# Performance work log

Hardware: AMD Instinct MI355X
Metric: run time of the kernel (lower is better)

Reference implementation:

```python
import jax, jax.numpy as jnp
import numpy as np

D_MODEL = 1024
N_HEADS = 16
HEAD_DIM = D_MODEL // N_HEADS
D_FF = 4 * D_MODEL
SEQ = 2048
BATCH = 2
EPS = 1e-6


def setup_inputs() -> dict:
    key = jax.random.key(0)
    ks = jax.random.split(key, 8)
    s = 0.02
    return {
        "x": jax.random.normal(ks[0], (SEQ, BATCH, D_MODEL), dtype=jnp.float32),
        "g1": jnp.ones((D_MODEL,), dtype=jnp.float32),                # norm1 weight
        "g2": jnp.ones((D_MODEL,), dtype=jnp.float32),                # norm2 weight
        "Wq": jax.random.normal(ks[1], (N_HEADS, D_MODEL, HEAD_DIM), dtype=jnp.float32) * s,
        "Wk": jax.random.normal(ks[2], (N_HEADS, D_MODEL, HEAD_DIM), dtype=jnp.float32) * s,
        "Wv": jax.random.normal(ks[3], (N_HEADS, D_MODEL, HEAD_DIM), dtype=jnp.float32) * s,
        "Wo": jax.random.normal(ks[4], (D_MODEL, D_MODEL), dtype=jnp.float32) * s,
        "W1": jax.random.normal(ks[5], (D_MODEL, D_FF), dtype=jnp.float32) * s,
        "W2": jax.random.normal(ks[6], (D_FF, D_MODEL), dtype=jnp.float32) * s,
    }


def _rmsnorm(x, g):
    rms = jnp.sqrt(jnp.mean(x * x, axis=-1, keepdims=True) + EPS)
    return g * (x / rms)


def _block(x, g1, g2, Wq, Wk, Wv, Wo, W1, W2):
    S = x.shape[0]
    scale = HEAD_DIM ** -0.5
    # --- attention (pre-norm) ---
    h = _rmsnorm(x, g1)                              # (S, B, D)
    Q = jnp.einsum('sbd,hdk->bhsk', h, Wq)           # (B, H, S, K)
    K = jnp.einsum('sbd,hdk->bhsk', h, Wk)
    V = jnp.einsum('sbd,hdk->bhsk', h, Wv)
    scores = jnp.einsum('bhsk,bhtk->bhst', Q, K) * scale
    causal = jnp.tril(jnp.ones((S, S), dtype=bool))
    scores = jnp.where(causal, scores, -jnp.inf)
    attn = jax.nn.softmax(scores, axis=-1)
    ctx = jnp.einsum('bhst,bhtk->sbhk', attn, V)     # heads concatenated in order
    ctx = ctx.reshape(S, x.shape[1], D_MODEL)
    x = x + ctx @ Wo
    # --- FFN (pre-norm) ---
    h2 = _rmsnorm(x, g2)
    x = x + jax.nn.silu(h2 @ W1) @ W2
    return x


def reference(x, g1, g2, Wq, Wk, Wv, Wo, W1, W2):
    return _block(x, g1, g2, Wq, Wk, Wv, Wo, W1, W2)
```

## Files before the change

### kernel.cpp

```cpp
#include <hip/hip_runtime.h>

typedef unsigned short u16;
typedef __bf16 bf16x8 __attribute__((ext_vector_type(8)));
typedef u16 u16x8 __attribute__((ext_vector_type(8)));
typedef u16 u16x4 __attribute__((ext_vector_type(4)));
typedef float f32x4 __attribute__((ext_vector_type(4)));

__device__ __forceinline__ u16 f2bf(float f) {
    union { float f; unsigned int u; } x; x.f = f;
    unsigned int r = x.u + 0x7FFFu + ((x.u >> 16) & 1u);
    return (u16)(r >> 16);
}

__device__ __forceinline__ u16 f2bf_hw(float f) {
    union { __bf16 b; u16 u; } x; x.b = (__bf16)f; return x.u;
}

__device__ __forceinline__ void gload_lds16(const u16* g, u16* l) {
    __builtin_amdgcn_global_load_lds(
        (const __attribute__((address_space(1))) unsigned int*)g,
        (__attribute__((address_space(3))) unsigned int*)l, 16, 0, 0);
}


__device__ __forceinline__ void transT_body(
    const float* __restrict__ in, u16* __restrict__ out, int R, int C,
    int bx, int by, float T[64][65], int tid)
{
    const int r0 = bx * 64, c0 = by * 64;
    const int tr = tid >> 4;
    const int tc = (tid & 15) * 4;
    #pragma unroll
    for (int k = 0; k < 4; k++) {
        f32x4 v = *(const f32x4*)(in + (size_t)(c0 + 16 * k + tr) * R + r0 + tc);
        T[16 * k + tr][tc]     = v[0];
        T[16 * k + tr][tc + 1] = v[1];
        T[16 * k + tr][tc + 2] = v[2];
        T[16 * k + tr][tc + 3] = v[3];
    }
    __syncthreads();
    #pragma unroll
    for (int k = 0; k < 4; k++) {
        const int rl = 16 * k + tr;
        u16x4 o;
        #pragma unroll
        for (int i = 0; i < 4; i++) o[i] = f2bf(T[tc + i][rl]);
        *(u16x4*)(out + (size_t)(r0 + rl) * C + c0 + tc) = o;
    }
}

__global__ __launch_bounds__(256) void prep_k(
    const float* __restrict__ Wq, const float* __restrict__ Wk,
    const float* __restrict__ Wv, const float* __restrict__ Wo,
    const float* __restrict__ W1, const float* __restrict__ W2,
    const float* __restrict__ x, const float* __restrict__ g1,
    u16* __restrict__ bqkvT, u16* __restrict__ woT,
    u16* __restrict__ w1T, u16* __restrict__ w2T, u16* __restrict__ h1)
{
    __shared__ float T[64][65];
    const int id = blockIdx.x;
    const int tid = threadIdx.x;

    if (id < 768) {
        const int bx = id & 15, y = id >> 4;
        const int d0 = bx * 64;
        const int wsel = y >> 4, h = y & 15;
        const float* W = (wsel == 0) ? Wq : (wsel == 1) ? Wk : Wv;
        const float scale = (wsel == 0) ? 0.125f * 1.44269504088896f : 1.0f;
        const int tr = tid >> 4;
        const int tc = (tid & 15) * 4;
        #pragma unroll
        for (int k = 0; k < 4; k++) {
            f32x4 v = *(const f32x4*)(W + (size_t)h * 65536 + (size_t)(d0 + 16 * k + tr) * 64 + tc);
            T[16 * k + tr][tc]     = v[0];
            T[16 * k + tr][tc + 1] = v[1];
            T[16 * k + tr][tc + 2] = v[2];
            T[16 * k + tr][tc + 3] = v[3];
        }
        __syncthreads();
        #pragma unroll
        for (int k = 0; k < 4; k++) {
            const int kk = 16 * k + tr;
            u16x4 o;
            #pragma unroll
            for (int i = 0; i < 4; i++) o[i] = f2bf(T[tc + i][kk] * scale);
            *(u16x4*)(bqkvT + (size_t)(wsel * 1024 + h * 64 + kk) * 1024 + d0 + tc) = o;
        }
    } else if (id < 1024) {
        const int id2 = id - 768;
        transT_body(Wo, woT, 1024, 1024, id2 & 15, id2 >> 4, T, tid);
    } else if (id < 2048) {
        const int id3 = id - 1024;
        transT_body(W1, w1T, 4096, 1024, id3 & 63, id3 >> 6, T, tid);
    } else if (id < 3072) {
        const int id4 = id - 2048;
        transT_body(W2, w2T, 1024, 4096, id4 & 15, id4 >> 4, T, tid);
    } else {
        const int row = id - 3072;
        const float* xr = x + (size_t)row * 1024;
        f32x4 v = *(const f32x4*)(xr + tid * 4);
        float ss = v[0] * v[0] + v[1] * v[1] + v[2] * v[2] + v[3] * v[3];
        #pragma unroll
        for (int off = 32; off > 0; off >>= 1) ss += __shfl_down(ss, off);
        float* red = &T[0][0];
        if ((tid & 63) == 0) red[tid >> 6] = ss;
        __syncthreads();
        float sum = red[0] + red[1] + red[2] + red[3];
        float rinv = rsqrtf(sum * (1.0f / 1024.0f) + 1e-6f);
        f32x4 gv = *(const f32x4*)(g1 + tid * 4);
        u16x4 o;
        #pragma unroll
        for (int i = 0; i < 4; i++) o[i] = f2bf(v[i] * gv[i] * rinv);
        *(u16x4*)(h1 + (size_t)row * 1024 + tid * 4) = o;
    }
}

__global__ __launch_bounds__(256) void vtrans_k(const u16* __restrict__ qkv, u16* __restrict__ vT)
{
    __shared__ u16 T[64][72];
    const int bh = blockIdx.x, b = bh >> 4, h = bh & 15;
    const int s0 = blockIdx.y * 64;
    const int tid = threadIdx.x;
    const int r = tid >> 2, c0 = (tid & 3) * 16;
    const u16* src = qkv + ((size_t)((s0 + r) * 2 + b)) * 3072 + 2048 + h * 64 + c0;
    *(u16x8*)&T[r][c0] = *(const u16x8*)src;
    *(u16x8*)&T[r][c0 + 8] = *(const u16x8*)(src + 8);
    __syncthreads();
    u16x8 o0, o1;
    #pragma unroll
    for (int i = 0; i < 8; i++) o0[i] = T[c0 + i][r];
    #pragma unroll
    for (int i = 0; i < 8; i++) o1[i] = T[c0 + 8 + i][r];
    u16* dst = vT + (size_t)(bh * 64 + r) * 2048 + s0 + c0;
    *(u16x8*)dst = o0;
    *(u16x8*)(dst + 8) = o1;
}

__global__ __launch_bounds__(256) void addred_norm_k(
    const float* __restrict__ res, const float* __restrict__ p0,
    const float* __restrict__ p1, const float* __restrict__ g,
    float* __restrict__ xout, u16* __restrict__ hout)
{
    const int row = blockIdx.x;
    const int tid = threadIdx.x;
    const size_t base = (size_t)row * 1024 + tid * 4;
    f32x4 a = *(const f32x4*)(res + base);
    f32x4 b = *(const f32x4*)(p0 + base);
    f32x4 c = *(const f32x4*)(p1 + base);
    f32x4 o = a + b + c;
    *(f32x4*)(xout + base) = o;
    float ss = o[0] * o[0] + o[1] * o[1] + o[2] * o[2] + o[3] * o[3];
    #pragma unroll
    for (int off = 32; off > 0; off >>= 1) ss += __shfl_down(ss, off);
    __shared__ float red[4];
    if ((tid & 63) == 0) red[tid >> 6] = ss;
    __syncthreads();
    float sum = red[0] + red[1] + red[2] + red[3];
    float rinv = rsqrtf(sum * (1.0f / 1024.0f) + 1e-6f);
    f32x4 gv = *(const f32x4*)(g + tid * 4);
    u16x4 hv;
    #pragma unroll
    for (int i = 0; i < 4; i++) hv[i] = f2bf(o[i] * gv[i] * rinv);
    *(u16x4*)(hout + base) = hv;
}

__global__ __launch_bounds__(256) void addredW_k(
    const float* __restrict__ a0, const float* __restrict__ a1,
    const float* __restrict__ a2, const float* __restrict__ a3,
    float* __restrict__ out)
{
    int i = (blockIdx.x * 256 + threadIdx.x) * 4;
    f32x4 v = *(const f32x4*)(a0 + i);
    v = v + *(const f32x4*)(a1 + i);
    v = v + *(const f32x4*)(a2 + i);
    v = v + *(const f32x4*)(a3 + i);
    *(f32x4*)(out + i) = v;
}

template <int MODE>
__global__ __launch_bounds__(256) void gemm_bt_k(
    const u16* __restrict__ A, const u16* __restrict__ BT,
    u16* __restrict__ outB, float* __restrict__ outF, const float* __restrict__ res,
    int M, int N, int K, int klen)
{
    __shared__ u16 As[2][128 * 64];
    __shared__ u16 Bs[2][128 * 64];
    const int tid = threadIdx.x;
    const int lane = tid & 63, w = tid >> 6;
    const int wm = w >> 1, wn = w & 1;
    const int quad = lane >> 4, l15 = lane & 15;
    const int bid = blockIdx.x + gridDim.x * blockIdx.y;
    const int bj = bid >> 3;
    const int m0 = ((bid & 7) * 4 + (bj & 3)) * 128;
    const int n0 = (bj >> 2) * 128;
    const int kbeg = blockIdx.z * klen;

    f32x4 acc[4][4] = {};

    const int srow = (w << 3) + (lane >> 3);
    const int swz = ((lane & 7) ^ (lane >> 3)) << 3;
    const u16* aA = A + (size_t)(m0 + srow) * K + kbeg + swz;
    const u16* aB = BT + (size_t)(n0 + srow) * K + kbeg + swz;
    const int wo = w * 512;
    const int rsw = (l15 & 7) << 3;

    #pragma unroll
    for (int c = 0; c < 4; c++) {
        gload_lds16(aA + (size_t)(c * 32) * K, &As[0][0] + c * 2048 + wo);
        gload_lds16(aB + (size_t)(c * 32) * K, &Bs[0][0] + c * 2048 + wo);
    }

    int cur = 0;
    for (int k0 = 0; k0 < klen; k0 += 64) {
        __syncthreads();
        if (k0 + 64 < klen) {
            #pragma unroll
            for (int c = 0; c < 4; c++) {
                gload_lds16(aA + (size_t)(c * 32) * K + k0 + 64, &As[cur ^ 1][0] + c * 2048 + wo);
                gload_lds16(aB + (size_t)(c * 32) * K + k0 + 64, &Bs[cur ^ 1][0] + c * 2048 + wo);
            }
        }
        const u16* AB = &As[cur][0];
        const u16* BB = &Bs[cur][0];
        #pragma unroll
        for (int kh = 0; kh < 2; kh++) {
            const int cb = ((kh * 4 + quad) << 3);
            bf16x8 af[4], bfr[4];
            #pragma unroll
            for (int i = 0; i < 4; i++)
                af[i] = *(const bf16x8*)(AB + (wm * 64 + i * 16 + l15) * 64 + (cb ^ rsw));
            #pragma unroll
            for (int j = 0; j < 4; j++)
                bfr[j] = *(const bf16x8*)(BB + (wn * 64 + j * 16 + l15) * 64 + (cb ^ rsw));
            #pragma unroll
            for (int i = 0; i < 4; i++)
                #pragma unroll
                for (int j = 0; j < 4; j++)
                    acc[i][j] = __builtin_amdgcn_mfma_f32_16x16x32_bf16(af[i], bfr[j], acc[i][j], 0, 0, 0);
        }
        cur ^= 1;
    }

    float* outFz = (MODE == 3) ? outF + (size_t)blockIdx.z * M * N : outF;
    #pragma unroll
    for (int i = 0; i < 4; i++) {
        const int row = m0 + wm * 64 + i * 16 + quad * 4;
        #pragma unroll
        for (int j = 0; j < 4; j++) {
            const int col = n0 + wn * 64 + j * 16 + l15;
            #pragma unroll
            for (int r = 0; r < 4; r++) {
                const size_t idx = (size_t)(row + r) * N + col;
                float v = acc[i][j][r];
                if (MODE == 0) {
                    outB[idx] = f2bf_hw(v);
                } else if (MODE == 1) {
                    outF[idx] = res[idx] + v;
                } else if (MODE == 2) {
                    float e = exp2f(v * -1.44269504088896f);
                    outB[idx] = f2bf_hw(v * __builtin_amdgcn_rcpf(1.0f + e));
                } else {
                    outFz[idx] = v;
                }
            }
        }
    }
}

#define MMQ(FH, AS, BS) \
    { _Pragma("unroll") \
      for (int i_ = 0; i_ < 4; i_++) { \
        acc[(FH)*4+i_][0] = __builtin_amdgcn_mfma_f32_16x16x32_bf16(AS[i_], BS[0], acc[(FH)*4+i_][0], 0, 0, 0); \
        acc[(FH)*4+i_][1] = __builtin_amdgcn_mfma_f32_16x16x32_bf16(AS[i_], BS[1], acc[(FH)*4+i_][1], 0, 0, 0); \
        acc[(FH)*4+i_][2] = __builtin_amdgcn_mfma_f32_16x16x32_bf16(AS[i_], BS[2], acc[(FH)*4+i_][2], 0, 0, 0); \
        acc[(FH)*4+i_][3] = __builtin_amdgcn_mfma_f32_16x16x32_bf16(AS[i_], BS[3], acc[(FH)*4+i_][3], 0, 0, 0); \
      } }

#define SBAR   __builtin_amdgcn_s_barrier()
#define FENCE  asm volatile("" ::: "memory")

template <int MODE>
__global__ __launch_bounds__(512, 2) void gemm8p_k(
    const u16* __restrict__ A, const u16* __restrict__ BT,
    u16* __restrict__ outB, float* __restrict__ q0, float* __restrict__ q1,
    float* __restrict__ q2, float* __restrict__ q3, const float* __restrict__ res,
    int N, int K, int klen)
{
    __shared__ u16 sm[65536];
    const int tid = threadIdx.x;
    const int lane = tid & 63, w = tid >> 6;
    const int l15 = lane & 15, quad = lane >> 4;
    const int wm = w >> 2, wn = w & 3;

    const int nwg = gridDim.x;
    const int bid = blockIdx.x;
    int m0, n0, kbeg, zz = 0;
    if (MODE == 3) {
        const int slot = bid >> 3;
        m0 = ((bid & 7) * 2 + (slot & 1)) * 256;
        n0 = ((slot >> 1) & 3) * 256;
        zz = slot >> 3;
        kbeg = zz * klen;
    } else {
        const int s = (bid & 7) * (nwg >> 3) + (bid >> 3);
        m0 = (s & 15) * 256;
        n0 = (s >> 4) * 256;
        kbeg = blockIdx.z * klen;
    }
    const int nT = klen >> 6;

    const int srow = w * 16 + (lane >> 2);
    const int scol = (((lane & 3) ^ ((lane >> 3) & 3)) << 3);
    const u16* gA = A + (size_t)(m0 + srow) * K + kbeg + scol;
    const u16* gB = BT + (size_t)(n0 + srow) * K + kbeg + scol;
    const size_t cstep = (size_t)128 * K;

    const int rswz = ((quad ^ ((l15 >> 1) & 3)) << 3);
    const int raoff = (wm * 128 + l15) * 32 + rswz;
    const int rboff = (wn * 64 + l15) * 32 + rswz;

    f32x4 acc[8][4] = {};

    auto stA = [&](int t, int kh) {
        u16* d = sm + (t & 1) * 32768 + kh * 8192 + w * 512;
        const u16* g = gA + (size_t)(t * 64 + kh * 32);
        gload_lds16(g, d);
        gload_lds16(g + cstep, d + 4096);
    };
    auto stB = [&](int t, int kh) {
        u16* d = sm + (t & 1) * 32768 + 16384 + kh * 8192 + w * 512;
        const u16* g = gB + (size_t)(t * 64 + kh * 32);
        gload_lds16(g, d);
        gload_lds16(g + cstep, d + 4096);
    };
    auto rdB = [&](int buf, int kh, bf16x8* b) {
        const u16* p = sm + buf * 32768 + 16384 + kh * 8192 + rboff;
        b[0] = *(const bf16x8*)(p);
        b[1] = *(const bf16x8*)(p + 512);
        b[2] = *(const bf16x8*)(p + 1024);
        b[3] = *(const bf16x8*)(p + 1536);
    };
    auto rdA = [&](int buf, int kh, int fh, bf16x8* a) {
        const u16* p = sm + buf * 32768 + kh * 8192 + fh * 2048 + raoff;
        a[0] = *(const bf16x8*)(p);
        a[1] = *(const bf16x8*)(p + 512);
        a[2] = *(const bf16x8*)(p + 1024);
        a[3] = *(const bf16x8*)(p + 1536);
    };

    stA(0, 0); stB(0, 0); stA(0, 1); stB(0, 1);
    if (nT > 1) {
        stA(1, 0); stB(1, 0);
        asm volatile("s_waitcnt vmcnt(4)" ::: "memory");
    } else {
        asm volatile("s_waitcnt vmcnt(0)" ::: "memory");
    }
    SBAR; FENCE;

    for (int t = 0; t < nT; t++) {
        const int buf = t & 1;
        bf16x8 a[4], b[4];
        rdA(buf, 0, 0, a); rdB(buf, 0, b);
        if (t + 1 < nT) stA(t + 1, 1);
        SBAR; FENCE;
        __builtin_amdgcn_s_setprio(1);
        MMQ(0, a, b)
        __builtin_amdgcn_s_setprio(0);
        SBAR; FENCE;
        rdA(buf, 0, 1, a);
        if (t + 1 < nT) stB(t + 1, 1);
        SBAR; FENCE;
        __builtin_amdgcn_s_setprio(1);
        MMQ(1, a, b)
        __builtin_amdgcn_s_setprio(0);
        SBAR; FENCE;
        rdA(buf, 1, 0, a); rdB(buf, 1, b);
        if (t + 2 < nT) stA(t + 2, 0);
        SBAR; FENCE;
        __builtin_amdgcn_s_setprio(1);
        MMQ(0, a, b)
        __builtin_amdgcn_s_setprio(0);
        SBAR; FENCE;
        rdA(buf, 1, 1, a);
        if (t + 2 < nT) {
            stB(t + 2, 0);
            asm volatile("s_waitcnt vmcnt(4)" ::: "memory");
        } else {
            asm volatile("s_waitcnt vmcnt(0)" ::: "memory");
        }
        SBAR; FENCE;
        __builtin_amdgcn_s_setprio(1);
        MMQ(1, a, b)
        __builtin_amdgcn_s_setprio(0);
        SBAR; FENCE;
    }

    float* po = nullptr;
    if (MODE == 3)
        po = (zz == 0) ? q0 : (zz == 1) ? q1 : (zz == 2) ? q2 : q3;
    #pragma unroll
    for (int mf = 0; mf < 8; mf++) {
        const int row = m0 + wm * 128 + mf * 16 + quad * 4;
        #pragma unroll
        for (int nf = 0; nf < 4; nf++) {
            const int col = n0 + wn * 64 + nf * 16 + l15;
            #pragma unroll
            for (int r = 0; r < 4; r++) {
                const size_t idx = (size_t)(row + r) * N + col;
                const float v = acc[mf][nf][r];
                if (MODE == 0) {
                    outB[idx] = f2bf_hw(v);
                } else if (MODE == 2) {
                    float e = exp2f(v * -1.44269504088896f);
                    outB[idx] = f2bf_hw(v * __builtin_amdgcn_rcpf(1.0f + e));
                } else {
                    po[idx] = (zz == 0) ? v + res[idx] : v;
                }
            }
        }
    }
}

__global__ __launch_bounds__(256, 4) void attn_k(const u16* __restrict__ qkv,
                                                 const u16* __restrict__ vT,
                                                 u16* __restrict__ ctx)
{
    const int bh = blockIdx.x;
    const int qt = 31 - (int)blockIdx.y;
    const int b = bh >> 4, h = bh & 15;
    const int q0 = qt * 64;
    const int tid = threadIdx.x;
    const int lane = tid & 63, w = tid >> 6;
    const int quad = lane >> 4, l15 = lane & 15;

    __shared__ u16 Ks[2][4096];
    __shared__ u16 Vs[2][4096];

    const int q = q0 + 16 * w + l15;
    const u16* qrow = qkv + ((size_t)(q * 2 + b)) * 3072 + h * 64;
    const bf16x8 aq0 = *(const bf16x8*)(qrow + quad * 8);
    const bf16x8 aq1 = *(const bf16x8*)(qrow + 32 + quad * 8);

    bf16x8 ones;
    #pragma unroll
    for (int i = 0; i < 8; i++) ones[i] = (__bf16)1.0f;

    const int kr = (w << 3) + (lane >> 3);
    const int swz = ((lane & 7) ^ (lane >> 3)) << 3;
    const int ldsoff = w * 512;
    const u16* kbase0 = qkv + ((size_t)(kr * 2 + b)) * 3072 + 1024 + h * 64 + swz;
    const u16* kbase1 = kbase0 + (size_t)32 * 2 * 3072;
    const u16* vrow0 = vT + (size_t)(bh * 64 + kr) * 2048 + swz;
    const u16* vrow1 = vrow0 + (size_t)32 * 2048;

    const int sl = (l15 & 3) | ((l15 & 4) << 1) | ((l15 & 8) >> 1);
    const int rswk = (sl & 7) << 3;
    const int rswv = (l15 & 7) << 3;
    const int sq = ((quad & 1) << 1) | (quad >> 1);
    const int qloc = 16 * w + l15;

    f32x4 o[4] = {};
    f32x4 accl = {};

    gload_lds16(kbase0, &Ks[0][0] + ldsoff);
    gload_lds16(kbase1, &Ks[0][0] + 2048 + ldsoff);
    gload_lds16(vrow0, &Vs[0][0] + ldsoff);
    gload_lds16(vrow1, &Vs[0][0] + 2048 + ldsoff);

    int cur = 0;
    for (int t0 = 0; t0 <= q0; t0 += 64) {
        __syncthreads();
        if (t0 + 64 <= q0) {
            const size_t go = (size_t)(t0 + 64) * 2 * 3072;
            u16* KB = &Ks[cur ^ 1][0];
            u16* VB = &Vs[cur ^ 1][0];
            gload_lds16(kbase0 + go, KB + ldsoff);
            gload_lds16(kbase1 + go, KB + 2048 + ldsoff);
            gload_lds16(vrow0 + (t0 + 64), VB + ldsoff);
            gload_lds16(vrow1 + (t0 + 64), VB + 2048 + ldsoff);
        }
        const u16* KB = &Ks[cur][0];
        const u16* VB = &Vs[cur][0];

        f32x4 s[4];
        __builtin_amdgcn_s_setprio(1);
        #pragma unroll
        for (int tg = 0; tg < 4; tg++) {
            const u16* kb = KB + (16 * tg + sl) * 64;
            bf16x8 ak0 = *(const bf16x8*)(kb + ((quad << 3) ^ rswk));
            bf16x8 ak1 = *(const bf16x8*)(kb + (((quad + 4) << 3) ^ rswk));
            f32x4 c = {};
            c = __builtin_amdgcn_mfma_f32_16x16x32_bf16(ak0, aq0, c, 0, 0, 0);
            c = __builtin_amdgcn_mfma_f32_16x16x32_bf16(ak1, aq1, c, 0, 0, 0);
            s[tg] = c;
        }
        __builtin_amdgcn_s_setprio(0);

        if (t0 == q0) {
            #pragma unroll
            for (int tg = 0; tg < 4; tg++)
                #pragma unroll
                for (int r = 0; r < 4; r++)
                    if ((16 * tg + 4 * sq + r) > qloc) s[tg][r] = -1e30f;
        }

        unsigned dd[4][2];
        #pragma unroll
        for (int tg = 0; tg < 4; tg++) {
            float e0 = exp2f(s[tg][0]), e1 = exp2f(s[tg][1]);
            float e2 = exp2f(s[tg][2]), e3 = exp2f(s[tg][3]);
            asm("v_cvt_pk_bf16_f32 %0, %1, %2" : "=v"(dd[tg][0]) : "v"(e0), "v"(e1));
            asm("v_cvt_pk_bf16_f32 %0, %1, %2" : "=v"(dd[tg][1]) : "v"(e2), "v"(e3));
        }
        unsigned x0 = dd[0][0], y0 = dd[1][0];
        asm volatile("v_permlane32_swap_b32 %0, %1" : "+v"(x0), "+v"(y0));
        unsigned x1 = dd[0][1], y1 = dd[1][1];
        asm volatile("v_permlane32_swap_b32 %0, %1" : "+v"(x1), "+v"(y1));
        unsigned x2 = dd[2][0], y2 = dd[3][0];
        asm volatile("v_permlane32_swap_b32 %0, %1" : "+v"(x2), "+v"(y2));
        unsigned x3 = dd[2][1], y3 = dd[3][1];
        asm volatile("v_permlane32_swap_b32 %0, %1" : "+v"(x3), "+v"(y3));

        union { unsigned u[4]; bf16x8 v; } pu0, pu1;
        pu0.u[0] = x0; pu0.u[1] = x1; pu0.u[2] = y0; pu0.u[3] = y1;
        pu1.u[0] = x2; pu1.u[1] = x3; pu1.u[2] = y2; pu1.u[3] = y3;
        const bf16x8 pf0 = pu0.v, pf1 = pu1.v;

        __builtin_amdgcn_s_setprio(1);
        accl = __builtin_amdgcn_mfma_f32_16x16x32_bf16(ones, pf0, accl, 0, 0, 0);
        accl = __builtin_amdgcn_mfma_f32_16x16x32_bf16(ones, pf1, accl, 0, 0, 0);
        #pragma unroll
        for (int i = 0; i < 4; i++) {
            const u16* vb = VB + (i * 16 + l15) * 64;
            bf16x8 av0 = *(const bf16x8*)(vb + ((quad << 3) ^ rswv));
            bf16x8 av1 = *(const bf16x8*)(vb + (((quad + 4) << 3) ^ rswv));
            o[i] = __builtin_amdgcn_mfma_f32_16x16x32_bf16(av0, pf0, o[i], 0, 0, 0);
            o[i] = __builtin_amdgcn_mfma_f32_16x16x32_bf16(av1, pf1, o[i], 0, 0, 0);
        }
        __builtin_amdgcn_s_setprio(0);
        cur ^= 1;
    }

    const float linv = 1.0f / accl[0];
    #pragma unroll
    for (int i = 0; i < 4; i++) {
        u16x4 ov;
        #pragma unroll
        for (int r = 0; r < 4; r++) ov[r] = f2bf_hw(o[i][r] * linv);
        *(u16x4*)(ctx + ((size_t)(q * 2 + b)) * 1024 + h * 64 + i * 16 + quad * 4) = ov;
    }
}

extern "C" void kernel_launch(void* const* d_in, const int* in_sizes, int n_in,
                              void* d_out, int out_size, void* d_ws, size_t ws_size,
                              hipStream_t stream)
{
    (void)in_sizes; (void)n_in; (void)out_size; (void)ws_size;
    const float* x  = (const float*)d_in[0];
    const float* g1 = (const float*)d_in[1];
    const float* g2 = (const float*)d_in[2];
    const float* Wq = (const float*)d_in[3];
    const float* Wk = (const float*)d_in[4];
    const float* Wv = (const float*)d_in[5];
    const float* Wo = (const float*)d_in[6];
    const float* W1 = (const float*)d_in[7];
    const float* W2 = (const float*)d_in[8];
    float* out = (float*)d_out;

    char* ws = (char*)d_ws;
    u16*   bqkvT = (u16*)(ws);
    u16*   woT   = (u16*)(ws + 6291456);
    u16*   w1T   = (u16*)(ws + 8388608);
    u16*   w2T   = (u16*)(ws + 16777216);
    u16*   h1    = (u16*)(ws + 25165824);
    u16*   qkvB  = (u16*)(ws + 33554432);
    u16*   vT    = (u16*)(ws + 25165824);
    u16*   ctxB  = (u16*)(ws + 58720256);
    float* xmid  = (float*)(ws + 41943040);
    u16*   h2    = (u16*)(ws + 83886080);
    u16*   actB  = (u16*)(ws + 92274688);
    float* partO = (float*)(ws + 92274688);
    float* p0 = (float*)(ws);
    float* p1 = (float*)(ws + 25165824);
    float* p2 = (float*)(ws + 58720256);
    float* p3 = (float*)(ws + 75497472);

    prep_k<<<7168, 256, 0, stream>>>(Wq, Wk, Wv, Wo, W1, W2, x, g1,
                                     bqkvT, woT, w1T, w2T, h1);

    gemm8p_k<0><<<dim3(192, 1, 1), 512, 0, stream>>>(h1, bqkvT, qkvB,
                                                     nullptr, nullptr, nullptr, nullptr,
                                                     nullptr, 3072, 1024, 1024);
    vtrans_k<<<dim3(32, 32), 256, 0, stream>>>(qkvB, vT);
    attn_k<<<dim3(32, 32), 256, 0, stream>>>(qkvB, vT, ctxB);

    gemm_bt_k<3><<<dim3(8, 32, 2), 256, 0, stream>>>(ctxB, woT, nullptr, partO, nullptr,
                                                     4096, 1024, 1024, 512);
    addred_norm_k<<<4096, 256, 0, stream>>>(x, partO, partO + 4096 * 1024, g2, xmid, h2);

    gemm8p_k<2><<<dim3(256, 1, 1), 512, 0, stream>>>(h2, w1T, actB,
                                                     nullptr, nullptr, nullptr, nullptr,
                                                     nullptr, 4096, 1024, 1024);
    gemm8p_k<3><<<dim3(256, 1, 1), 512, 0, stream>>>(actB, w2T, nullptr,
                                                     p0, p1, p2, p3,
                                                     xmid, 1024, 4096, 1024);
    addredW_k<<<4096 * 1024 / 1024, 256, 0, stream>>>(p0, p1, p2, p3, out);
}
```

Before: 335.6 us.

## Drop split-K for Wo GEMM with fused residual and restructure W2 grid

The Wo projection now runs as a single-pass GEMM (mode 1) that adds the residual x directly into xmid. This removes the two-way split-K partials and the combined add-reduce-norm kernel; a plain RMSNorm kernel then produces h2. The W2 GEMM's split-K tile mapping moves from a custom block-id decode to a 64x4 grid using blockIdx.z. The Wo GEMM loses some parallelism in exchange for less partial-sum traffic, and the W2 block ordering changes, which may affect L2 locality.

```diff
diff --git a/kernel.cpp b/kernel.cpp
--- a/kernel.cpp
+++ b/kernel.cpp
@@ -115,6 +115,28 @@
     }
 }
 
+__global__ __launch_bounds__(256) void rmsnorm_k(
+    const float* __restrict__ x, const float* __restrict__ g, u16* __restrict__ out)
+{
+    const int row = blockIdx.x;
+    const int tid = threadIdx.x;
+    const float* xr = x + (size_t)row * 1024;
+    f32x4 v = *(const f32x4*)(xr + tid * 4);
+    float ss = v[0] * v[0] + v[1] * v[1] + v[2] * v[2] + v[3] * v[3];
+    #pragma unroll
+    for (int off = 32; off > 0; off >>= 1) ss += __shfl_down(ss, off);
+    __shared__ float red[4];
+    if ((tid & 63) == 0) red[tid >> 6] = ss;
+    __syncthreads();
+    float sum = red[0] + red[1] + red[2] + red[3];
+    float rinv = rsqrtf(sum * (1.0f / 1024.0f) + 1e-6f);
+    f32x4 gv = *(const f32x4*)(g + tid * 4);
+    u16x4 o;
+    #pragma unroll
+    for (int i = 0; i < 4; i++) o[i] = f2bf(v[i] * gv[i] * rinv);
+    *(u16x4*)(out + (size_t)row * 1024 + tid * 4) = o;
+}
+
 __global__ __launch_bounds__(256) void vtrans_k(const u16* __restrict__ qkv, u16* __restrict__ vT)
 {
     __shared__ u16 T[64][72];
@@ -134,34 +156,6 @@
     u16* dst = vT + (size_t)(bh * 64 + r) * 2048 + s0 + c0;
     *(u16x8*)dst = o0;
     *(u16x8*)(dst + 8) = o1;
-}
-
-__global__ __launch_bounds__(256) void addred_norm_k(
-    const float* __restrict__ res, const float* __restrict__ p0,
-    const float* __restrict__ p1, const float* __restrict__ g,
-    float* __restrict__ xout, u16* __restrict__ hout)
-{
-    const int row = blockIdx.x;
-    const int tid = threadIdx.x;
-    const size_t base = (size_t)row * 1024 + tid * 4;
-    f32x4 a = *(const f32x4*)(res + base);
-    f32x4 b = *(const f32x4*)(p0 + base);
-    f32x4 c = *(const f32x4*)(p1 + base);
-    f32x4 o = a + b + c;
-    *(f32x4*)(xout + base) = o;
-    float ss = o[0] * o[0] + o[1] * o[1] + o[2] * o[2] + o[3] * o[3];
-    #pragma unroll
-    for (int off = 32; off > 0; off >>= 1) ss += __shfl_down(ss, off);
-    __shared__ float red[4];
-    if ((tid & 63) == 0) red[tid >> 6] = ss;
-    __syncthreads();
-    float sum = red[0] + red[1] + red[2] + red[3];
-    float rinv = rsqrtf(sum * (1.0f / 1024.0f) + 1e-6f);
-    f32x4 gv = *(const f32x4*)(g + tid * 4);
-    u16x4 hv;
-    #pragma unroll
-    for (int i = 0; i < 4; i++) hv[i] = f2bf(o[i] * gv[i] * rinv);
-    *(u16x4*)(hout + base) = hv;
 }
 
 __global__ __launch_bounds__(256) void addredW_k(
@@ -294,19 +288,11 @@
 
     const int nwg = gridDim.x;
     const int bid = blockIdx.x;
-    int m0, n0, kbeg, zz = 0;
-    if (MODE == 3) {
-        const int slot = bid >> 3;
-        m0 = ((bid & 7) * 2 + (slot & 1)) * 256;
-        n0 = ((slot >> 1) & 3) * 256;
-        zz = slot >> 3;
-        kbeg = zz * klen;
-    } else {
-        const int s = (bid & 7) * (nwg >> 3) + (bid >> 3);
-        m0 = (s & 15) * 256;
-        n0 = (s >> 4) * 256;
-        kbeg = blockIdx.z * klen;
-    }
+    const int s = (bid & 7) * (nwg >> 3) + (bid >> 3);
+    const int m0 = (s & 15) * 256;
+    const int n0 = (s >> 4) * 256;
+    const int zz = blockIdx.z;
+    const int kbeg = zz * klen;
     const int nT = klen >> 6;
 
     const int srow = w * 16 + (lane >> 2);
@@ -579,7 +565,6 @@
     float* xmid  = (float*)(ws + 41943040);
     u16*   h2    = (u16*)(ws + 83886080);
     u16*   actB  = (u16*)(ws + 92274688);
-    float* partO = (float*)(ws + 92274688);
     float* p0 = (float*)(ws);
     float* p1 = (float*)(ws + 25165824);
     float* p2 = (float*)(ws + 58720256);
@@ -594,15 +579,15 @@
     vtrans_k<<<dim3(32, 32), 256, 0, stream>>>(qkvB, vT);
     attn_k<<<dim3(32, 32), 256, 0, stream>>>(qkvB, vT, ctxB);
 
-    gemm_bt_k<3><<<dim3(8, 32, 2), 256, 0, stream>>>(ctxB, woT, nullptr, partO, nullptr,
-                                                     4096, 1024, 1024, 512);
-    addred_norm_k<<<4096, 256, 0, stream>>>(x, partO, partO + 4096 * 1024, g2, xmid, h2);
+    gemm_bt_k<1><<<dim3(8, 32), 256, 0, stream>>>(ctxB, woT, nullptr, xmid, x,
+                                                  4096, 1024, 1024, 1024);
+    rmsnorm_k<<<4096, 256, 0, stream>>>(xmid, g2, h2);
 
     gemm8p_k<2><<<dim3(256, 1, 1), 512, 0, stream>>>(h2, w1T, actB,
                                                      nullptr, nullptr, nullptr, nullptr,
                                                      nullptr, 4096, 1024, 1024);
-    gemm8p_k<3><<<dim3(256, 1, 1), 512, 0, stream>>>(actB, w2T, nullptr,
-                                                     p0, p1, p2, p3,
-                                                     xmid, 1024, 4096, 1024);
+    gemm8p_k<3><<<dim3(64, 1, 4), 512, 0, stream>>>(actB, w2T, nullptr,
+                                                    p0, p1, p2, p3,
+                                                    xmid, 1024, 4096, 1024);
     addredW_k<<<4096 * 1024 / 1024, 256, 0, stream>>>(p0, p1, p2, p3, out);
 }
```

After: 334.7 us. About the same (-0.3%).
